# Performance work log

Measured on AMD Instinct MI355X. Metric: run time of the kernel, lower is better.

Reference implementation:

```python
import jax, jax.numpy as jnp
import numpy as np

B, L, D, V, S, R = 4096, 128, 100, 800000, 1024, 512
EPS = 1e-5

def setup_inputs() -> dict:
    key = jax.random.key(0)
    ks = jax.random.split(key, 10)
    bound = float(np.sqrt(6.0 / D))
    return {
        "statement_vecs": jax.random.normal(ks[0], (B, S), jnp.float32),
        "qa_ids": jax.random.randint(ks[1], (B, L, 2), 0, V),
        "qa_lens": jax.random.randint(ks[2], (B,), 0, L + 1),
        "emb": jax.random.uniform(ks[3], (V, D), jnp.float32, -bound, bound),
        "W1": jax.random.normal(ks[4], (2 * D + S, 2 * R), jnp.float32) * 0.02,
        "b1": jnp.zeros((2 * R,), jnp.float32),
        "g1": jnp.ones((2 * R,), jnp.float32),
        "beta1": jnp.zeros((2 * R,), jnp.float32),
        "W2": jax.random.normal(ks[5], (2 * R, R), jnp.float32) * 0.02,
        "b2": jnp.zeros((R,), jnp.float32),
        "g2": jnp.ones((R,), jnp.float32),
        "beta2": jnp.zeros((R,), jnp.float32),
        "W3": jax.random.normal(ks[6], (R, 1), jnp.float32) * 0.02,
        "b3": jnp.zeros((1,), jnp.float32),
    }

def _batchnorm(x, g, b):
    # BatchNorm1d in training mode: biased batch statistics over batch dim
    m = x.mean(0)
    v = ((x - m) ** 2).mean(0)
    return (x - m) * jax.lax.rsqrt(v + EPS) * g + b

def reference(statement_vecs, qa_ids, qa_lens, emb, W1, b1, g1, beta1, W2, b2, g2, beta2, W3, b3):
    # ragged mean-pool of (L_i, 2, D) concept embeddings, zero vector if length 0
    mask = (jnp.arange(L)[None, :] < qa_lens[:, None]).astype(emb.dtype)  # [B, L]
    qa_embed = emb[qa_ids]                                                # [B, L, 2, D]
    denom = jnp.maximum(qa_lens, 1).astype(emb.dtype)                     # avoid /0 (sum is 0 then)
    qa_pooled = (qa_embed * mask[:, :, None, None]).sum(1) / denom[:, None, None]  # [B, 2, D]
    qa_pooled = qa_pooled.reshape(B, 2 * D)
    qas = jnp.concatenate([qa_pooled, statement_vecs], axis=1)            # [B, 2D+S]
    # relation_extractor: Linear -> ReLU -> BN -> Linear -> BN -> ReLU
    h = _batchnorm(jax.nn.relu(qas @ W1 + b1), g1, beta1)
    h = jax.nn.relu(_batchnorm(h @ W2 + b2, g2, beta2))
    logits = h @ W3 + b3                                                  # [B, 1]
    return logits
```

## Files before the change

kernel.cpp:

```cpp
#include <hip/hip_runtime.h>
#include <hip/hip_bf16.h>

#define B_ 4096
#define L_ 128
#define D_ 100
#define S_ 1024
#define R_ 512
#define K1P_ 1280
#define N1_ 1024
#define EPS_ 1e-5f
#define NW1BLK_ (32 * (K1P_ / 32))

typedef short bf16x8 __attribute__((ext_vector_type(8)));
typedef short short4v __attribute__((ext_vector_type(4)));
typedef float f32x4 __attribute__((ext_vector_type(4)));

static __device__ __forceinline__ short f2bf(float x) {
  union { float f; unsigned u; } c; c.f = x;
  unsigned r = (c.u + 0x7fffu + ((c.u >> 16) & 1u)) >> 16;
  return (short)r;
}
static __device__ __forceinline__ float bf2f(short x) {
  union { unsigned u; float f; } c; c.u = ((unsigned)(unsigned short)x) << 16;
  return c.f;
}

__global__ __launch_bounds__(256) void prep_kernel(
    const float* __restrict__ sv, const int* __restrict__ qa_ids,
    const int* __restrict__ qa_lens, const float* __restrict__ emb,
    const float* __restrict__ W1, short* __restrict__ qas,
    short* __restrict__ W1t) {
  int t = threadIdx.x;
  if (blockIdx.x < NW1BLK_) {
    __shared__ float tile[32][33];
    int bx = blockIdx.x;
    int n0 = (bx & 31) * 32, k0 = (bx >> 5) * 32;
#pragma unroll
    for (int p = 0; p < 4; ++p) {
      int kk = (t >> 5) + p * 8, nn = t & 31;
      int k = k0 + kk;
      tile[kk][nn] = (k < 1224) ? W1[(size_t)k * N1_ + n0 + nn] : 0.f;
    }
    __syncthreads();
#pragma unroll
    for (int p = 0; p < 4; ++p) {
      int nn = (t >> 5) + p * 8, kk = t & 31;
      W1t[(size_t)(n0 + nn) * K1P_ + k0 + kk] = f2bf(tile[kk][nn]);
    }
  } else {
    int b = blockIdx.x - NW1BLK_;
    __shared__ int ids[L_ * 2];
    __shared__ __align__(16) float partial[4][2][D_];
    int len = qa_lens[b];
    ids[t] = qa_ids[(size_t)b * (L_ * 2) + t];
    __syncthreads();
    int w = t >> 6, l = t & 63;
    int rs = l >> 5;
    int li = l & 31;
    if (li < 25) {
      float4 a0 = {0.f, 0.f, 0.f, 0.f}, a1 = {0.f, 0.f, 0.f, 0.f};
      int n2 = 2 * len;
      int r = 2 * w + rs;
      for (; r + 8 < n2; r += 16) {
        const float* row0 = emb + (size_t)ids[r] * D_;
        const float* row1 = emb + (size_t)ids[r + 8] * D_;
        float4 v0 = *reinterpret_cast<const float4*>(row0 + li * 4);
        float4 v1 = *reinterpret_cast<const float4*>(row1 + li * 4);
        a0.x += v0.x; a0.y += v0.y; a0.z += v0.z; a0.w += v0.w;
        a1.x += v1.x; a1.y += v1.y; a1.z += v1.z; a1.w += v1.w;
      }
      if (r < n2) {
        const float* row0 = emb + (size_t)ids[r] * D_;
        float4 v0 = *reinterpret_cast<const float4*>(row0 + li * 4);
        a0.x += v0.x; a0.y += v0.y; a0.z += v0.z; a0.w += v0.w;
      }
      a0.x += a1.x; a0.y += a1.y; a0.z += a1.z; a0.w += a1.w;
      *reinterpret_cast<float4*>(&partial[w][rs][li * 4]) = a0;
    }
    __syncthreads();
    short* qrow = qas + (size_t)b * K1P_;
    if (t < 200) {
      int k = t / 100, d = t - k * 100;
      float s = partial[0][k][d] + partial[1][k][d] +
                partial[2][k][d] + partial[3][k][d];
      qrow[t] = f2bf(s / (float)(len > 0 ? len : 1));
    }
    {
      float4 v = *reinterpret_cast<const float4*>(sv + (size_t)b * S_ + t * 4);
      short4v o;
      o[0] = f2bf(v.x); o[1] = f2bf(v.y); o[2] = f2bf(v.z); o[3] = f2bf(v.w);
      *(short4v*)&qrow[200 + t * 4] = o;
    }
    if (t < K1P_ - 1224) qrow[1224 + t] = 0;
  }
}

template <int ROWS>
static __device__ __forceinline__ void stage_tile64(
    const short* __restrict__ gp, int stride, int k0, short* lds, int t) {
#pragma unroll
  for (int p = 0; p < ROWS / 32; ++p) {
    int off16 = p * 256 + t;
    int r = off16 >> 3;
    int c = off16 & 7;
    int kc = c ^ (r & 7);
    const short* g = gp + (size_t)r * stride + k0 + kc * 8;
    __builtin_amdgcn_global_load_lds(
        (const __attribute__((address_space(1))) void*)g,
        (__attribute__((address_space(3))) void*)(lds + (size_t)off16 * 8),
        16, 0, 0);
  }
}

template <int BM, int BN, int WM, int WN, bool RELU, int NBIAS, int NX, int NY>
__global__ __launch_bounds__(256) void mfma_gemm(
    const short* __restrict__ A, const short* __restrict__ Bt,
    const float* __restrict__ biasp, short* __restrict__ C,
    float* __restrict__ part, int K, int N) {
  constexpr int FM = BM / WM / 16;
  constexpr int FN = BN / WN / 16;
  __shared__ short As[2][BM * 64];
  __shared__ short Bs[2][BN * 64];
  __shared__ float sred[WM][WN][FN][16];
  __shared__ float qred[WM][WN][FN][16];
  const int t = threadIdx.x;
  const int l = t & 63, w = t >> 6;
  const int wr = w / WN, wc = w % WN;
  constexpr int CPX = NX * NY / 8;
  const int bid = blockIdx.x;
  const int swz = (bid & 7) * CPX + (bid >> 3);
  const int bxx = swz % NX, byy = swz / NX;
  const int row0 = byy * BM, col0 = bxx * BN;
  const short* Ab = A + (size_t)row0 * K;
  const short* Bb = Bt + (size_t)col0 * K;
  f32x4 acc[FM][FN] = {};
  const int lrow = l & 15, lkc = l >> 4;
  const int nt = K / 64;
  stage_tile64<BM>(Ab, K, 0, As[0], t);
  stage_tile64<BN>(Bb, K, 0, Bs[0], t);
  __syncthreads();
  for (int ts = 0; ts < nt; ++ts) {
    const int cur = ts & 1;
    if (ts + 1 < nt) {
      stage_tile64<BM>(Ab, K, (ts + 1) * 64, As[cur ^ 1], t);
      stage_tile64<BN>(Bb, K, (ts + 1) * 64, Bs[cur ^ 1], t);
    }
    bf16x8 af[2][FM], bfr[2][FN];
#pragma unroll
    for (int ks = 0; ks < 2; ++ks) {
#pragma unroll
      for (int m = 0; m < FM; ++m) {
        int r = wr * (BM / WM) + m * 16 + lrow;
        int ch = (ks * 4 + lkc) ^ (r & 7);
        af[ks][m] = *(const bf16x8*)&As[cur][r * 64 + ch * 8];
      }
#pragma unroll
      for (int n = 0; n < FN; ++n) {
        int r = wc * (BN / WN) + n * 16 + lrow;
        int ch = (ks * 4 + lkc) ^ (r & 7);
        bfr[ks][n] = *(const bf16x8*)&Bs[cur][r * 64 + ch * 8];
      }
    }
#pragma unroll
    for (int ks = 0; ks < 2; ++ks)
#pragma unroll
      for (int m = 0; m < FM; ++m)
#pragma unroll
        for (int n = 0; n < FN; ++n)
          acc[m][n] = __builtin_amdgcn_mfma_f32_16x16x32_bf16(
              af[ks][m], bfr[ks][n], acc[m][n], 0, 0, 0);
    __syncthreads();
  }
  float bvn[FN];
#pragma unroll
  for (int n = 0; n < FN; ++n) {
    int col = col0 + wc * (BN / WN) + n * 16 + lrow;
    float bv = 0.f;
#pragma unroll
    for (int i = 0; i < NBIAS; ++i) bv += biasp[(size_t)i * N + col];
    bvn[n] = bv;
  }
  float ss[FN], qq[FN];
#pragma unroll
  for (int n = 0; n < FN; ++n) { ss[n] = 0.f; qq[n] = 0.f; }
#pragma unroll
  for (int m = 0; m < FM; ++m) {
#pragma unroll
    for (int n = 0; n < FN; ++n) {
      int col = col0 + wc * (BN / WN) + n * 16 + lrow;
#pragma unroll
      for (int j = 0; j < 4; ++j) {
        int row = row0 + wr * (BM / WM) + m * 16 + (l >> 4) * 4 + j;
        float v = acc[m][n][j] + bvn[n];
        if (RELU) v = fmaxf(v, 0.f);
        short vb = f2bf(v);
        C[(size_t)row * N + col] = vb;
        float f = bf2f(vb);
        ss[n] += f;
        qq[n] += f * f;
      }
    }
  }
#pragma unroll
  for (int n = 0; n < FN; ++n) {
    ss[n] += __shfl_xor(ss[n], 16);
    ss[n] += __shfl_xor(ss[n], 32);
    qq[n] += __shfl_xor(qq[n], 16);
    qq[n] += __shfl_xor(qq[n], 32);
  }
  if (l < 16) {
#pragma unroll
    for (int n = 0; n < FN; ++n) {
      sred[wr][wc][n][l] = ss[n];
      qred[wr][wc][n][l] = qq[n];
    }
  }
  __syncthreads();
  if (t < WN * FN * 16) {
    int c16 = t & 15, n = (t >> 4) % FN, wcc = t / (16 * FN);
    float s = 0.f, q = 0.f;
#pragma unroll
    for (int r = 0; r < WM; ++r) { s += sred[r][wcc][n][c16]; q += qred[r][wcc][n][c16]; }
    int col = col0 + wcc * (BN / WN) + n * 16 + c16;
    part[(size_t)byy * 2 * N + col] = s;
    part[(size_t)byy * 2 * N + N + col] = q;
  }
}

__global__ __launch_bounds__(256) void fold_tile(
    const float* __restrict__ part1, const float* __restrict__ W2,
    const float* __restrict__ b2, const float* __restrict__ g1,
    const float* __restrict__ beta1, short* __restrict__ W2pt,
    float* __restrict__ pbias) {
  int kt = blockIdx.x, jt = blockIdx.y;
  int t = threadIdx.x;
  int k0 = kt * 64, j0 = jt * 64;
  __shared__ float a1s[64], c1s[64];
  __shared__ float tT[64][65];
  __shared__ float bred[16][64];
  if (t < 64) {
    float s = 0.f, q = 0.f;
    for (int b = 0; b < 32; ++b) {
      s += part1[(size_t)b * 2048 + k0 + t];
      q += part1[(size_t)b * 2048 + 1024 + k0 + t];
    }
    float mean = s * (1.f / B_);
    float var = q * (1.f / B_) - mean * mean;
    float a = g1[k0 + t] * rsqrtf(var + EPS_);
    a1s[t] = a;
    c1s[t] = beta1[k0 + t] - mean * a;
  }
  __syncthreads();
  int g = t >> 4, j4 = t & 15;
  float pb0 = 0.f, pb1 = 0.f, pb2 = 0.f, pb3 = 0.f;
#pragma unroll
  for (int p = 0; p < 4; ++p) {
    int kk = g + p * 16;
    float4 wv = *(const float4*)&W2[(size_t)(k0 + kk) * R_ + j0 + j4 * 4];
    float a = a1s[kk], cc = c1s[kk];
    tT[j4 * 4 + 0][kk] = a * wv.x;
    tT[j4 * 4 + 1][kk] = a * wv.y;
    tT[j4 * 4 + 2][kk] = a * wv.z;
    tT[j4 * 4 + 3][kk] = a * wv.w;
    pb0 += cc * wv.x; pb1 += cc * wv.y; pb2 += cc * wv.z; pb3 += cc * wv.w;
  }
  bred[g][j4 * 4 + 0] = pb0;
  bred[g][j4 * 4 + 1] = pb1;
  bred[g][j4 * 4 + 2] = pb2;
  bred[g][j4 * 4 + 3] = pb3;
  __syncthreads();
#pragma unroll
  for (int p = 0; p < 4; ++p) {
    int jj = g + p * 16;
    short4v o;
    o[0] = f2bf(tT[jj][j4 * 4 + 0]);
    o[1] = f2bf(tT[jj][j4 * 4 + 1]);
    o[2] = f2bf(tT[jj][j4 * 4 + 2]);
    o[3] = f2bf(tT[jj][j4 * 4 + 3]);
    *(short4v*)&W2pt[(size_t)(j0 + jj) * N1_ + k0 + j4 * 4] = o;
  }
  if (t < 64) {
    float pbv = 0.f;
#pragma unroll
    for (int gg = 0; gg < 16; ++gg) pbv += bred[gg][t];
    if (kt == 0) pbv += b2[j0 + t];
    pbias[(size_t)kt * R_ + j0 + t] = pbv;
  }
}

__global__ __launch_bounds__(256) void reduce_bn2(
    const float* __restrict__ part2, const float* __restrict__ g2,
    const float* __restrict__ beta2, float* __restrict__ a2c2) {
  int j = blockIdx.x * 256 + threadIdx.x;
  if (j >= R_) return;
  float s = 0.f, q = 0.f;
  for (int b = 0; b < 64; ++b) {
    s += part2[(size_t)b * 1024 + j];
    q += part2[(size_t)b * 1024 + 512 + j];
  }
  float mean = s * (1.f / B_);
  float var = q * (1.f / B_) - mean * mean;
  float a = g2[j] * rsqrtf(var + EPS_);
  a2c2[j] = a;
  a2c2[R_ + j] = beta2[j] - mean * a;
}

__global__ __launch_bounds__(256) void final_kernel(
    const short* __restrict__ z2, const float* __restrict__ a2c2,
    const float* __restrict__ W3, const float* __restrict__ b3,
    float* __restrict__ out) {
  int wave = threadIdx.x >> 6;
  int lane = threadIdx.x & 63;
  int row = blockIdx.x * 4 + wave;
  const short* zr = z2 + (size_t)row * R_;
  int j0 = lane * 8;
  bf16x8 zv = *(const bf16x8*)&zr[j0];
  float acc = 0.f;
#pragma unroll
  for (int i = 0; i < 8; ++i) {
    float h = fmaxf(bf2f(zv[i]) * a2c2[j0 + i] + a2c2[R_ + j0 + i], 0.f);
    acc += h * W3[j0 + i];
  }
  for (int off = 32; off > 0; off >>= 1) acc += __shfl_down(acc, off, 64);
  if (lane == 0) out[row] = acc + b3[0];
}

extern "C" void kernel_launch(void* const* d_in, const int* in_sizes, int n_in,
                              void* d_out, int out_size, void* d_ws, size_t ws_size,
                              hipStream_t stream) {
  const float* sv      = (const float*)d_in[0];
  const int*   qa_ids  = (const int*)d_in[1];
  const int*   qa_lens = (const int*)d_in[2];
  const float* emb     = (const float*)d_in[3];
  const float* W1      = (const float*)d_in[4];
  const float* b1      = (const float*)d_in[5];
  const float* g1      = (const float*)d_in[6];
  const float* beta1   = (const float*)d_in[7];
  const float* W2      = (const float*)d_in[8];
  const float* b2      = (const float*)d_in[9];
  const float* g2      = (const float*)d_in[10];
  const float* beta2   = (const float*)d_in[11];
  const float* W3      = (const float*)d_in[12];
  const float* b3      = (const float*)d_in[13];
  float* out = (float*)d_out;

  char* p = (char*)d_ws;
  short* qas    = (short*)p; p += (size_t)B_ * K1P_ * 2;
  short* W1t    = (short*)p; p += (size_t)N1_ * K1P_ * 2;
  short* h1     = (short*)p; p += (size_t)B_ * N1_ * 2;
  short* W2pt   = (short*)p; p += (size_t)R_ * N1_ * 2;
  short* z2     = (short*)p; p += (size_t)B_ * R_ * 2;
  float* pbias  = (float*)p; p += (size_t)16 * R_ * 4;
  float* a2c2   = (float*)p; p += 2 * R_ * 4;
  float* part1  = (float*)p; p += (size_t)32 * 2 * N1_ * 4;
  float* part2  = (float*)p;

  prep_kernel<<<NW1BLK_ + B_, 256, 0, stream>>>(
      sv, qa_ids, qa_lens, emb, W1, qas, W1t);
  mfma_gemm<128, 64, 2, 2, true, 1, 16, 32>
      <<<512, 256, 0, stream>>>(qas, W1t, b1, h1, part1, K1P_, N1_);
  fold_tile<<<dim3(16, 8), 256, 0, stream>>>(part1, W2, b2, g1, beta1, W2pt, pbias);
  mfma_gemm<64, 64, 2, 2, false, 16, 8, 64>
      <<<512, 256, 0, stream>>>(h1, W2pt, pbias, z2, part2, N1_, R_);
  reduce_bn2<<<2, 256, 0, stream>>>(part2, g2, beta2, a2c2);
  final_kernel<<<B_ / 4, 256, 0, stream>>>(z2, a2c2, W3, b3, out);
}
```

Baseline: 97.90 us.

## Fuse statement-vector bf16 conversion into first GEMM's A-tile loading

The prep kernel no longer converts statement_vecs into a bf16 staging buffer. A new first-layer GEMM kernel reads the fp32 statement vectors directly, converts them to bf16 in registers and writes swizzled LDS tiles. It then stages the small pooled-embedding buffer (padded to 256) for the last K tiles. W1 is permuted so its K order matches this new layout. The aim is to drop the round trip of writing and re-reading the large bf16 activation buffer, at the cost of register-staged A loads replacing the async global-to-LDS copies for most K steps.

```diff
diff --git a/kernel.cpp b/kernel.cpp
--- a/kernel.cpp
+++ b/kernel.cpp
@@ -6,6 +6,7 @@
 #define D_ 100
 #define S_ 1024
 #define R_ 512
+#define KP_ 256
 #define K1P_ 1280
 #define N1_ 1024
 #define EPS_ 1e-5f
@@ -26,10 +27,9 @@
 }
 
 __global__ __launch_bounds__(256) void prep_kernel(
-    const float* __restrict__ sv, const int* __restrict__ qa_ids,
-    const int* __restrict__ qa_lens, const float* __restrict__ emb,
-    const float* __restrict__ W1, short* __restrict__ qas,
-    short* __restrict__ W1t) {
+    const int* __restrict__ qa_ids, const int* __restrict__ qa_lens,
+    const float* __restrict__ emb, const float* __restrict__ W1,
+    short* __restrict__ qas_p, short* __restrict__ W1t) {
   int t = threadIdx.x;
   if (blockIdx.x < NW1BLK_) {
     __shared__ float tile[32][33];
@@ -45,7 +45,9 @@
 #pragma unroll
     for (int p = 0; p < 4; ++p) {
       int nn = (t >> 5) + p * 8, kk = t & 31;
-      W1t[(size_t)(n0 + nn) * K1P_ + k0 + kk] = f2bf(tile[kk][nn]);
+      int k = k0 + kk;
+      int nk = (k < 200) ? 1024 + k : (k < 1224 ? k - 200 : k);
+      W1t[(size_t)(n0 + nn) * K1P_ + nk] = f2bf(tile[kk][nn]);
     }
   } else {
     int b = blockIdx.x - NW1BLK_;
@@ -78,20 +80,15 @@
       *reinterpret_cast<float4*>(&partial[w][rs][li * 4]) = a0;
     }
     __syncthreads();
-    short* qrow = qas + (size_t)b * K1P_;
+    short* qrow = qas_p + (size_t)b * KP_;
     if (t < 200) {
       int k = t / 100, d = t - k * 100;
       float s = partial[0][k][d] + partial[1][k][d] +
                 partial[2][k][d] + partial[3][k][d];
       qrow[t] = f2bf(s / (float)(len > 0 ? len : 1));
-    }
-    {
-      float4 v = *reinterpret_cast<const float4*>(sv + (size_t)b * S_ + t * 4);
-      short4v o;
-      o[0] = f2bf(v.x); o[1] = f2bf(v.y); o[2] = f2bf(v.z); o[3] = f2bf(v.w);
-      *(short4v*)&qrow[200 + t * 4] = o;
-    }
-    if (t < K1P_ - 1224) qrow[1224 + t] = 0;
+    } else if (t < KP_) {
+      qrow[t] = 0;
+    }
   }
 }
 
@@ -109,6 +106,139 @@
         (const __attribute__((address_space(1))) void*)g,
         (__attribute__((address_space(3))) void*)(lds + (size_t)off16 * 8),
         16, 0, 0);
+  }
+}
+
+template <int NX, int NY>
+__global__ __launch_bounds__(256) void gemm1_kernel(
+    const float* __restrict__ sv, const short* __restrict__ qas_p,
+    const short* __restrict__ W1t, const float* __restrict__ b1,
+    short* __restrict__ h1, float* __restrict__ part) {
+  __shared__ short As[2][128 * 64];
+  __shared__ short Bs[2][64 * 64];
+  __shared__ float sred[2][2][2][16];
+  __shared__ float qred[2][2][2][16];
+  const int t = threadIdx.x;
+  const int l = t & 63, w = t >> 6;
+  const int wr = w >> 1, wc = w & 1;
+  constexpr int CPX = NX * NY / 8;
+  const int bid = blockIdx.x;
+  const int swz = (bid & 7) * CPX + (bid >> 3);
+  const int bxx = swz % NX, byy = swz / NX;
+  const int row0 = byy * 128, col0 = bxx * 64;
+  f32x4 acc[4][2] = {};
+  const int lrow = l & 15, lkc = l >> 4;
+  float4 ra[4], rb[4];
+  auto loadA = [&](int k0) {
+#pragma unroll
+    for (int p = 0; p < 4; ++p) {
+      int idx = p * 256 + t;
+      int r = idx >> 3, c = idx & 7;
+      const float* g = sv + (size_t)(row0 + r) * S_ + k0 + c * 8;
+      ra[p] = *reinterpret_cast<const float4*>(g);
+      rb[p] = *reinterpret_cast<const float4*>(g + 4);
+    }
+  };
+  auto writeA = [&](short* dst) {
+#pragma unroll
+    for (int p = 0; p < 4; ++p) {
+      int idx = p * 256 + t;
+      int r = idx >> 3, c = idx & 7;
+      int ch = c ^ (r & 7);
+      bf16x8 v;
+      v[0] = f2bf(ra[p].x); v[1] = f2bf(ra[p].y);
+      v[2] = f2bf(ra[p].z); v[3] = f2bf(ra[p].w);
+      v[4] = f2bf(rb[p].x); v[5] = f2bf(rb[p].y);
+      v[6] = f2bf(rb[p].z); v[7] = f2bf(rb[p].w);
+      *(bf16x8*)&dst[r * 64 + ch * 8] = v;
+    }
+  };
+  const short* Aq = qas_p + (size_t)row0 * KP_;
+  const short* Bb = W1t + (size_t)col0 * K1P_;
+  auto stageB = [&](int k0, short* dst) { stage_tile64<64>(Bb, K1P_, k0, dst, t); };
+  loadA(0);
+  stageB(0, Bs[0]);
+  writeA(As[0]);
+  __syncthreads();
+  const int nt = 20;
+  for (int ts = 0; ts < nt; ++ts) {
+    const int cur = ts & 1;
+    if (ts + 1 < nt) {
+      if (ts + 1 < 16) loadA((ts + 1) * 64);
+      else stage_tile64<128>(Aq, KP_, (ts + 1 - 16) * 64, As[cur ^ 1], t);
+      stageB((ts + 1) * 64, Bs[cur ^ 1]);
+    }
+    bf16x8 af[2][4], bfr[2][2];
+#pragma unroll
+    for (int ks = 0; ks < 2; ++ks) {
+#pragma unroll
+      for (int m = 0; m < 4; ++m) {
+        int r = wr * 64 + m * 16 + lrow;
+        int ch = (ks * 4 + lkc) ^ (r & 7);
+        af[ks][m] = *(const bf16x8*)&As[cur][r * 64 + ch * 8];
+      }
+#pragma unroll
+      for (int n = 0; n < 2; ++n) {
+        int r = wc * 32 + n * 16 + lrow;
+        int ch = (ks * 4 + lkc) ^ (r & 7);
+        bfr[ks][n] = *(const bf16x8*)&Bs[cur][r * 64 + ch * 8];
+      }
+    }
+#pragma unroll
+    for (int ks = 0; ks < 2; ++ks)
+#pragma unroll
+      for (int m = 0; m < 4; ++m)
+#pragma unroll
+        for (int n = 0; n < 2; ++n)
+          acc[m][n] = __builtin_amdgcn_mfma_f32_16x16x32_bf16(
+              af[ks][m], bfr[ks][n], acc[m][n], 0, 0, 0);
+    if (ts + 1 < nt && ts + 1 < 16) writeA(As[cur ^ 1]);
+    __syncthreads();
+  }
+  float bvn[2];
+#pragma unroll
+  for (int n = 0; n < 2; ++n) bvn[n] = b1[col0 + wc * 32 + n * 16 + lrow];
+  float ss[2] = {}, qq[2] = {};
+#pragma unroll
+  for (int m = 0; m < 4; ++m) {
+#pragma unroll
+    for (int n = 0; n < 2; ++n) {
+      int col = col0 + wc * 32 + n * 16 + lrow;
+#pragma unroll
+      for (int j = 0; j < 4; ++j) {
+        int row = row0 + wr * 64 + m * 16 + (l >> 4) * 4 + j;
+        float v = fmaxf(acc[m][n][j] + bvn[n], 0.f);
+        short vb = f2bf(v);
+        h1[(size_t)row * N1_ + col] = vb;
+        float f = bf2f(vb);
+        ss[n] += f;
+        qq[n] += f * f;
+      }
+    }
+  }
+#pragma unroll
+  for (int n = 0; n < 2; ++n) {
+    ss[n] += __shfl_xor(ss[n], 16);
+    ss[n] += __shfl_xor(ss[n], 32);
+    qq[n] += __shfl_xor(qq[n], 16);
+    qq[n] += __shfl_xor(qq[n], 32);
+  }
+  if (l < 16) {
+#pragma unroll
+    for (int n = 0; n < 2; ++n) {
+      sred[wr][wc][n][l] = ss[n];
+      qred[wr][wc][n][l] = qq[n];
+    }
+  }
+  __syncthreads();
+  if (t < 64) {
+    int c16 = t & 15, n = (t >> 4) & 1, wcc = t >> 5;
+    float s = 0.f, q = 0.f;
+#pragma unroll
+    for (int r = 0; r < 2; ++r) { s += sred[r][wcc][n][c16]; q += qred[r][wcc][n][c16]; }
+    int col = col0 + wcc * 32 + n * 16 + c16;
+    part[(size_t)byy * 2 * N1_ + col] = s;
+    part[(size_t)byy * 2 * N1_ + N1_ + col] = q;
   }
 }
 
@@ -345,7 +475,7 @@
   float* out = (float*)d_out;
 
   char* p = (char*)d_ws;
-  short* qas    = (short*)p; p += (size_t)B_ * K1P_ * 2;
+  short* qas_p  = (short*)p; p += (size_t)B_ * KP_ * 2;
   short* W1t    = (short*)p; p += (size_t)N1_ * K1P_ * 2;
   short* h1     = (short*)p; p += (size_t)B_ * N1_ * 2;
   short* W2pt   = (short*)p; p += (size_t)R_ * N1_ * 2;
@@ -355,10 +485,8 @@
   float* part1  = (float*)p; p += (size_t)32 * 2 * N1_ * 4;
   float* part2  = (float*)p;
 
-  prep_kernel<<<NW1BLK_ + B_, 256, 0, stream>>>(
-      sv, qa_ids, qa_lens, emb, W1, qas, W1t);
-  mfma_gemm<128, 64, 2, 2, true, 1, 16, 32>
-      <<<512, 256, 0, stream>>>(qas, W1t, b1, h1, part1, K1P_, N1_);
+  prep_kernel<<<NW1BLK_ + B_, 256, 0, stream>>>(qa_ids, qa_lens, emb, W1, qas_p, W1t);
+  gemm1_kernel<16, 32><<<512, 256, 0, stream>>>(sv, qas_p, W1t, b1, h1, part1);
   fold_tile<<<dim3(16, 8), 256, 0, stream>>>(part1, W2, b2, g1, beta1, W2pt, pbias);
   mfma_gemm<64, 64, 2, 2, false, 16, 8, 64>
       <<<512, 256, 0, stream>>>(h1, W2pt, pbias, z2, part2, N1_, R_);
```

New measurement: 102.1 us. 1.04x slower.
